# Performance work log

Measured on AMD Instinct MI355X. Metric: run time of the kernel, lower is better.

Reference implementation:

```python
import jax, jax.numpy as jnp
import numpy as np

ALP = 0.1
LAM = 1.0
N_NODES = 100000
N_EDGES = 800000
D_FEAT = 64


def setup_inputs() -> dict:
    key = jax.random.key(0)
    ks = jax.random.split(key, 7)
    h = jax.random.normal(ks[0], (N_NODES, D_FEAT), dtype=jnp.float32)
    ini_h = jax.random.normal(ks[1], (N_NODES, D_FEAT), dtype=jnp.float32)
    bef_A = jax.random.uniform(ks[2], (N_NODES, 1), dtype=jnp.float32)
    aft_A = jax.random.uniform(ks[3], (N_NODES, 1), dtype=jnp.float32)
    bef_X = jax.random.uniform(ks[4], (N_NODES, 1), dtype=jnp.float32)
    src = jax.random.randint(ks[5], (N_EDGES,), 0, N_NODES, dtype=jnp.int32)
    dst = jax.random.randint(ks[6], (N_EDGES,), 0, N_NODES, dtype=jnp.int32)
    return {"h": h, "ini_h": ini_h, "bef_A": bef_A, "aft_A": aft_A,
            "bef_X": bef_X, "src": src, "dst": dst}


def reference(h, ini_h, bef_A, aft_A, bef_X, src, dst):
    # propagation_lt:
    #   ini_h' = ini_h * bef_X
    #   agg    = A @ (h * aft_A)   (copy_u/sum over edges src->dst)
    #   out    = alp*lam * (agg * bef_A) + (1-alp)*h + alp*ini_h'
    pre_h = h
    msg = (h * aft_A)[src]                                  # [E, D]
    agg = jax.ops.segment_sum(msg, dst, num_segments=N_NODES)  # [N, D]
    agg = agg * bef_A
    return ALP * LAM * agg + (1.0 - ALP) * pre_h + ALP * (ini_h * bef_X)
```

## Files before the change

### kernel.cpp

```cpp
#include <hip/hip_runtime.h>

#define ALP 0.1f
#define OMA 0.9f
#define D 64
#define DV 16
#define SH 7
#define NODES_PER_B 128
#define NBMAX 1024
#define CAP 16
#define OVF_MAX 65536

__device__ __forceinline__ unsigned short f2b(float f) {
    unsigned u = __float_as_uint(f);
    unsigned r = u + 0x7fffu + ((u >> 16) & 1u);
    return (unsigned short)(r >> 16);
}
__device__ __forceinline__ float b2f(unsigned short u) {
    return __uint_as_float(((unsigned)u) << 16);
}

__global__ __launch_bounds__(256) void vsgc_msgp1(
        const float4* __restrict__ h4, const float* __restrict__ aft_A,
        ushort4* __restrict__ msgb, int n16,
        const int4* __restrict__ src4, const int4* __restrict__ dst4,
        int* __restrict__ gcnt, int* __restrict__ buckets,
        int2* __restrict__ ovf, int* __restrict__ ovfCnt,
        int E, int NB, int BCAP, int p1Blocks) {
    int tid = threadIdx.x;
    if ((int)blockIdx.x >= p1Blocks) {
        int i = (blockIdx.x - p1Blocks) * 256 + tid;
        if (i < n16) {
            float w = aft_A[i >> 4];
            float4 v = h4[i];
            msgb[i] = make_ushort4(f2b(v.x * w), f2b(v.y * w), f2b(v.z * w), f2b(v.w * w));
        }
        return;
    }
    __shared__ int cnt[NBMAX], gbase[NBMAX], pos[NBMAX];
#pragma unroll
    for (int j = 0; j < NBMAX / 256; ++j) { cnt[tid + j * 256] = 0; pos[tid + j * 256] = 0; }
    __syncthreads();
    int nInt4 = (E + 3) >> 2;
    int i0 = blockIdx.x * 512 + tid;
    int i1 = i0 + 256;
    bool v0 = i0 < nInt4, v1 = i1 < nInt4;
    int4 s0 = make_int4(0,0,0,0), d0 = s0, s1 = s0, d1 = s0;
    if (v0) { s0 = src4[i0]; d0 = dst4[i0]; }
    if (v1) { s1 = src4[i1]; d1 = dst4[i1]; }
    int e0 = i0 << 2, e1 = i1 << 2;
    int ss[8] = {s0.x, s0.y, s0.z, s0.w, s1.x, s1.y, s1.z, s1.w};
    int dd[8] = {d0.x, d0.y, d0.z, d0.w, d1.x, d1.y, d1.z, d1.w};
    bool ok[8];
#pragma unroll
    for (int k = 0; k < 4; ++k) { ok[k] = v0 && (e0 + k < E); ok[4 + k] = v1 && (e1 + k < E); }
#pragma unroll
    for (int k = 0; k < 8; ++k) if (ok[k]) atomicAdd(&cnt[dd[k] >> SH], 1);
    __syncthreads();
    for (int bb = tid; bb < NB; bb += 256)
        if (cnt[bb] > 0) gbase[bb] = atomicAdd(&gcnt[bb], cnt[bb]);
    __syncthreads();
    int pp[8];
#pragma unroll
    for (int k = 0; k < 8; ++k)
        pp[k] = ok[k] ? (gbase[dd[k] >> SH] + atomicAdd(&pos[dd[k] >> SH], 1)) : 0;
#pragma unroll
    for (int k = 0; k < 8; ++k) {
        if (!ok[k]) continue;
        int b = dd[k] >> SH;
        int pkt = (ss[k] << SH) | (dd[k] & (NODES_PER_B - 1));
        if (pp[k] < BCAP) buckets[(size_t)b * BCAP + pp[k]] = pkt;
        else { int o = atomicAdd(ovfCnt, 1); if (o < OVF_MAX) ovf[o] = make_int2(ss[k], dd[k]); }
    }
}

__global__ __launch_bounds__(512) void p2_gather(
        const int* __restrict__ buckets, const int* __restrict__ gcnt,
        const ushort4* __restrict__ msgb,
        const float4* __restrict__ h4, const float4* __restrict__ ini4,
        const float* __restrict__ bef_A, const float* __restrict__ bef_X,
        int2* __restrict__ ovf, int* __restrict__ ovfCnt,
        float4* __restrict__ out4, int N, int BCAP) {
    __shared__ int npos[NODES_PER_B];
    __shared__ int ells[NODES_PER_B * CAP];
    int b = blockIdx.x, tid = threadIdx.x;
    if (tid < NODES_PER_B) npos[tid] = 0;
    __syncthreads();
    int nb = min(gcnt[b], BCAP);
    const int4* bp4 = (const int4*)(buckets + (size_t)b * BCAP);
    int nIter = (nb + 3) >> 2;
    for (int i4 = tid; i4 < nIter; i4 += 512) {
        int4 r4 = bp4[i4];
        int base = i4 << 2;
        int pk[4] = {r4.x, r4.y, r4.z, r4.w};
#pragma unroll
        for (int k = 0; k < 4; ++k) {
            if (base + k >= nb) break;
            int pkt = pk[k];
            int l = pkt & (NODES_PER_B - 1);
            int s = (int)(((unsigned)pkt) >> SH);
            int slot = atomicAdd(&npos[l], 1);
            if (slot < CAP) ells[l * CAP + slot] = s;
            else { int o = atomicAdd(ovfCnt, 1); if (o < OVF_MAX) ovf[o] = make_int2(s, (b << SH) + l); }
        }
    }
    __syncthreads();
    int lane = tid & 63;
    int wv = tid >> 6;
    int w = lane >> 4;
    int q = lane & 15;
    int node0 = b << SH;
    unsigned clampN = (unsigned)(N - 1);
    for (int pair = wv; pair < NODES_PER_B / 2; pair += 8) {
        int l0 = pair * 2;
        int g0 = node0 + l0;
        if (g0 >= N) break;
        int g1 = g0 + 1;
        bool has1 = g1 < N;
        int l1c = has1 ? (l0 + 1) : l0;
        int g1c = node0 + l1c;
        size_t r0 = (size_t)g0 * DV + q;
        size_t r1 = (size_t)g1c * DV + q;
        int ev0 = ells[l0 * CAP + q];
        int ev1 = ells[l1c * CAP + q];
        int n0 = min(npos[l0], CAP);
        int n1 = has1 ? min(npos[l1c], CAP) : 0;
        float4 hv0 = h4[r0];
        float4 hv1 = h4[r1];
        float4 iv0 = ini4[r0];
        float4 iv1 = ini4[r1];
        float cb0 = ALP * bef_A[g0];
        float bx0 = ALP * bef_X[g0];
        float cb1 = ALP * bef_A[g1c];
        float bx1 = ALP * bef_X[g1c];
        float4 a0 = make_float4(0.f, 0.f, 0.f, 0.f);
        float4 a1 = a0;
#pragma unroll
        for (int k = 0; k < 4; ++k) {
            int idx = w + 4 * k;
            int s0 = __shfl(ev0, idx);
            int s1 = __shfl(ev1, idx);
            unsigned su0 = min((unsigned)s0, clampN);
            unsigned su1 = min((unsigned)s1, clampN);
            float m0 = (idx < n0) ? 1.f : 0.f;
            float m1 = (idx < n1) ? 1.f : 0.f;
            ushort4 q0 = msgb[(size_t)su0 * DV + q];
            ushort4 q1 = msgb[(size_t)su1 * DV + q];
            a0.x += m0 * b2f(q0.x); a0.y += m0 * b2f(q0.y);
            a0.z += m0 * b2f(q0.z); a0.w += m0 * b2f(q0.w);
            a1.x += m1 * b2f(q1.x); a1.y += m1 * b2f(q1.y);
            a1.z += m1 * b2f(q1.z); a1.w += m1 * b2f(q1.w);
        }
        a0.x += __shfl_xor(a0.x, 16); a0.y += __shfl_xor(a0.y, 16);
        a0.z += __shfl_xor(a0.z, 16); a0.w += __shfl_xor(a0.w, 16);
        a0.x += __shfl_xor(a0.x, 32); a0.y += __shfl_xor(a0.y, 32);
        a0.z += __shfl_xor(a0.z, 32); a0.w += __shfl_xor(a0.w, 32);
        a1.x += __shfl_xor(a1.x, 16); a1.y += __shfl_xor(a1.y, 16);
        a1.z += __shfl_xor(a1.z, 16); a1.w += __shfl_xor(a1.w, 16);
        a1.x += __shfl_xor(a1.x, 32); a1.y += __shfl_xor(a1.y, 32);
        a1.z += __shfl_xor(a1.z, 32); a1.w += __shfl_xor(a1.w, 32);
        if (w == 0) {
            float4 o;
            o.x = OMA * hv0.x + bx0 * iv0.x + cb0 * a0.x;
            o.y = OMA * hv0.y + bx0 * iv0.y + cb0 * a0.y;
            o.z = OMA * hv0.z + bx0 * iv0.z + cb0 * a0.z;
            o.w = OMA * hv0.w + bx0 * iv0.w + cb0 * a0.w;
            out4[r0] = o;
        } else if (w == 1 && has1) {
            float4 o;
            o.x = OMA * hv1.x + bx1 * iv1.x + cb1 * a1.x;
            o.y = OMA * hv1.y + bx1 * iv1.y + cb1 * a1.y;
            o.z = OMA * hv1.z + bx1 * iv1.z + cb1 * a1.z;
            o.w = OMA * hv1.w + bx1 * iv1.w + cb1 * a1.w;
            out4[r1] = o;
        }
    }
}

__global__ void vsgc_ovf(const float4* __restrict__ h4,
                         const float* __restrict__ aft_A,
                         const float* __restrict__ bef_A,
                         const int2* __restrict__ ovf,
                         const int* __restrict__ ovfCnt,
                         float* __restrict__ out) {
    int total = min(*ovfCnt, OVF_MAX);
    int stride = blockDim.x * gridDim.x;
    for (int t = blockIdx.x * blockDim.x + threadIdx.x; t < total * 16; t += stride) {
        int e = t >> 4, q = t & 15;
        int2 r = ovf[e];
        float c = ALP * aft_A[r.x] * bef_A[r.y];
        float4 hv = h4[(size_t)r.x * DV + q];
        float* op = out + (size_t)r.y * D + (q << 2);
        unsafeAtomicAdd(op + 0, c * hv.x);
        unsafeAtomicAdd(op + 1, c * hv.y);
        unsafeAtomicAdd(op + 2, c * hv.z);
        unsafeAtomicAdd(op + 3, c * hv.w);
    }
}

__global__ void vsgc_init(const float4* __restrict__ h, const float4* __restrict__ ini_h,
                          const float* __restrict__ bef_X, float4* __restrict__ out, int n4) {
    int i = blockIdx.x * blockDim.x + threadIdx.x;
    if (i >= n4) return;
    int node = i >> 4;
    float bx = ALP * bef_X[node];
    float4 hv = h[i];
    float4 iv = ini_h[i];
    float4 o;
    o.x = OMA * hv.x + bx * iv.x;
    o.y = OMA * hv.y + bx * iv.y;
    o.z = OMA * hv.z + bx * iv.z;
    o.w = OMA * hv.w + bx * iv.w;
    out[i] = o;
}
__global__ void vsgc_edges_atomic(const float4* __restrict__ h,
                                  const float* __restrict__ aft_A,
                                  const float* __restrict__ bef_A,
                                  const int* __restrict__ src,
                                  const int* __restrict__ dst,
                                  float* __restrict__ out, int E) {
    int tid = blockIdx.x * blockDim.x + threadIdx.x;
    int e = tid >> 4;
    int q = tid & 15;
    if (e >= E) return;
    int s = src[e];
    int d = dst[e];
    float c = ALP * aft_A[s] * bef_A[d];
    float4 hv = h[(size_t)s * DV + q];
    float* op = out + (size_t)d * D + (q << 2);
    unsafeAtomicAdd(op + 0, c * hv.x);
    unsafeAtomicAdd(op + 1, c * hv.y);
    unsafeAtomicAdd(op + 2, c * hv.z);
    unsafeAtomicAdd(op + 3, c * hv.w);
}

extern "C" void kernel_launch(void* const* d_in, const int* in_sizes, int n_in,
                              void* d_out, int out_size, void* d_ws, size_t ws_size,
                              hipStream_t stream) {
    const float* h     = (const float*)d_in[0];
    const float* ini_h = (const float*)d_in[1];
    const float* bef_A = (const float*)d_in[2];
    const float* aft_A = (const float*)d_in[3];
    const float* bef_X = (const float*)d_in[4];
    const int*   src   = (const int*)d_in[5];
    const int*   dst   = (const int*)d_in[6];
    float* out = (float*)d_out;

    const int N = in_sizes[0] / D;
    const int E = in_sizes[5];
    const int t = 256;

    int NB = (N + NODES_PER_B - 1) >> SH;
    int perB = (NB > 0) ? E / NB : 0;
    int BCAP = ((perB + perB / 4 + 256) + 3) & ~3;

    size_t o_gcnt = 0;
    size_t o_ovfc = NBMAX * 4;
    size_t o_ovf  = ((o_ovfc + 64 * 4 + 255) / 256) * 256;
    size_t o_bkt  = ((o_ovf + (size_t)OVF_MAX * 8 + 255) / 256) * 256;
    size_t o_msg  = ((o_bkt + (size_t)NB * BCAP * 4 + 255) / 256) * 256;
    size_t need   = o_msg + (size_t)N * 128;

    if (NB <= NBMAX && N <= (1 << (31 - SH)) && ws_size >= need) {
        int*  gcnt  = (int*)((char*)d_ws + o_gcnt);
        int*  ovfC  = (int*)((char*)d_ws + o_ovfc);
        int2* ovf   = (int2*)((char*)d_ws + o_ovf);
        int*  bkt   = (int*)((char*)d_ws + o_bkt);
        ushort4* msgb = (ushort4*)((char*)d_ws + o_msg);

        hipMemsetAsync(d_ws, 0, o_ovf, stream);

        int n16 = N * DV;
        int nInt4 = (E + 3) >> 2;
        int p1Blocks = (nInt4 + 511) / 512;
        int msgBlocks = (n16 + t - 1) / t;
        vsgc_msgp1<<<p1Blocks + msgBlocks, t, 0, stream>>>(
            (const float4*)h, aft_A, msgb, n16,
            (const int4*)src, (const int4*)dst, gcnt, bkt, ovf, ovfC,
            E, NB, BCAP, p1Blocks);

        p2_gather<<<NB, 512, 0, stream>>>(
            bkt, gcnt, msgb, (const float4*)h, (const float4*)ini_h,
            bef_A, bef_X, ovf, ovfC, (float4*)out, N, BCAP);

        vsgc_ovf<<<32, t, 0, stream>>>((const float4*)h, aft_A, bef_A, ovf, ovfC, out);
    } else {
        int n4 = N * DV;
        vsgc_init<<<(n4 + t - 1) / t, t, 0, stream>>>(
            (const float4*)h, (const float4*)ini_h, bef_X, (float4*)out, n4);
        long long total = (long long)E * DV;
        vsgc_edges_atomic<<<(int)((total + t - 1) / t), t, 0, stream>>>(
            (const float4*)h, aft_A, bef_A, src, dst, out, E);
    }
}
```

Before: 164.7 us.

## Fuse bucketing, gather and overflow passes into one cooperative persistent kernel

Replaces the memset plus three kernel launches with a single cooperative kernel that uses grid-wide syncs between phases: zeroing counters, edge bucketing, bf16 message conversion, per-bucket gather and the overflow fixup. Blocks loop persistently over edge chunks and buckets. The aim is to remove launch gaps and the memset. In exchange, the grid is capped by occupancy (at most 1024 blocks), blocks shrink from 512 to 256 threads, and the bucketing now handles 4 edges per thread per iteration, with block-level syncs inside each iteration.

```diff
diff --git a/kernel.cpp b/kernel.cpp
--- a/kernel.cpp
+++ b/kernel.cpp
@@ -1,4 +1,7 @@
 #include <hip/hip_runtime.h>
+#include <hip/hip_cooperative_groups.h>
+
+namespace cg = cooperative_groups;
 
 #define ALP 0.1f
 #define OMA 0.9f
@@ -19,181 +22,189 @@
     return __uint_as_float(((unsigned)u) << 16);
 }
 
-__global__ __launch_bounds__(256) void vsgc_msgp1(
-        const float4* __restrict__ h4, const float* __restrict__ aft_A,
-        ushort4* __restrict__ msgb, int n16,
+__global__ __launch_bounds__(256, 4) void vsgc_all(
+        const float4* __restrict__ h4, const float4* __restrict__ ini4,
+        const float* __restrict__ bef_A, const float* __restrict__ aft_A,
+        const float* __restrict__ bef_X,
         const int4* __restrict__ src4, const int4* __restrict__ dst4,
+        float4* __restrict__ out4, ushort4* __restrict__ msgb,
         int* __restrict__ gcnt, int* __restrict__ buckets,
         int2* __restrict__ ovf, int* __restrict__ ovfCnt,
-        int E, int NB, int BCAP, int p1Blocks) {
+        int N, int E, int NB, int BCAP, int n16, int nInt4) {
+    __shared__ int smraw[3 * NBMAX];
+    cg::grid_group grid = cg::this_grid();
     int tid = threadIdx.x;
-    if ((int)blockIdx.x >= p1Blocks) {
-        int i = (blockIdx.x - p1Blocks) * 256 + tid;
-        if (i < n16) {
+    int G = gridDim.x;
+
+    if (blockIdx.x == 0) {
+        for (int i = tid; i < NBMAX; i += 256) gcnt[i] = 0;
+        if (tid == 0) *ovfCnt = 0;
+    }
+    grid.sync();
+
+    {
+        int* cnt   = smraw;
+        int* gbase = smraw + NBMAX;
+        int* pos   = smraw + 2 * NBMAX;
+        for (int base4 = blockIdx.x * 256; base4 < nInt4; base4 += G * 256) {
+#pragma unroll
+            for (int j = 0; j < NBMAX / 256; ++j) { cnt[tid + j * 256] = 0; pos[tid + j * 256] = 0; }
+            __syncthreads();
+            int i4 = base4 + tid;
+            bool v = i4 < nInt4;
+            int4 sv = make_int4(0, 0, 0, 0), dv = sv;
+            if (v) { sv = src4[i4]; dv = dst4[i4]; }
+            int e0 = i4 << 2;
+            int ss[4] = {sv.x, sv.y, sv.z, sv.w};
+            int dd[4] = {dv.x, dv.y, dv.z, dv.w};
+            bool ok[4];
+#pragma unroll
+            for (int k = 0; k < 4; ++k) ok[k] = v && (e0 + k < E);
+#pragma unroll
+            for (int k = 0; k < 4; ++k) if (ok[k]) atomicAdd(&cnt[dd[k] >> SH], 1);
+            __syncthreads();
+            for (int bb = tid; bb < NB; bb += 256)
+                if (cnt[bb] > 0) gbase[bb] = atomicAdd(&gcnt[bb], cnt[bb]);
+            __syncthreads();
+            int pp[4];
+#pragma unroll
+            for (int k = 0; k < 4; ++k)
+                pp[k] = ok[k] ? (gbase[dd[k] >> SH] + atomicAdd(&pos[dd[k] >> SH], 1)) : 0;
+#pragma unroll
+            for (int k = 0; k < 4; ++k) {
+                if (!ok[k]) continue;
+                int b = dd[k] >> SH;
+                int pkt = (ss[k] << SH) | (dd[k] & (NODES_PER_B - 1));
+                if (pp[k] < BCAP) buckets[(size_t)b * BCAP + pp[k]] = pkt;
+                else { int o = atomicAdd(ovfCnt, 1); if (o < OVF_MAX) ovf[o] = make_int2(ss[k], dd[k]); }
+            }
+            __syncthreads();
+        }
+    }
+    {
+        int stride = G * 256;
+        for (int i = blockIdx.x * 256 + tid; i < n16; i += stride) {
             float w = aft_A[i >> 4];
-            float4 v = h4[i];
-            msgb[i] = make_ushort4(f2b(v.x * w), f2b(v.y * w), f2b(v.z * w), f2b(v.w * w));
+            float4 vv = h4[i];
+            msgb[i] = make_ushort4(f2b(vv.x * w), f2b(vv.y * w), f2b(vv.z * w), f2b(vv.w * w));
         }
-        return;
-    }
-    __shared__ int cnt[NBMAX], gbase[NBMAX], pos[NBMAX];
-#pragma unroll
-    for (int j = 0; j < NBMAX / 256; ++j) { cnt[tid + j * 256] = 0; pos[tid + j * 256] = 0; }
-    __syncthreads();
-    int nInt4 = (E + 3) >> 2;
-    int i0 = blockIdx.x * 512 + tid;
-    int i1 = i0 + 256;
-    bool v0 = i0 < nInt4, v1 = i1 < nInt4;
-    int4 s0 = make_int4(0,0,0,0), d0 = s0, s1 = s0, d1 = s0;
-    if (v0) { s0 = src4[i0]; d0 = dst4[i0]; }
-    if (v1) { s1 = src4[i1]; d1 = dst4[i1]; }
-    int e0 = i0 << 2, e1 = i1 << 2;
-    int ss[8] = {s0.x, s0.y, s0.z, s0.w, s1.x, s1.y, s1.z, s1.w};
-    int dd[8] = {d0.x, d0.y, d0.z, d0.w, d1.x, d1.y, d1.z, d1.w};
-    bool ok[8];
-#pragma unroll
-    for (int k = 0; k < 4; ++k) { ok[k] = v0 && (e0 + k < E); ok[4 + k] = v1 && (e1 + k < E); }
-#pragma unroll
-    for (int k = 0; k < 8; ++k) if (ok[k]) atomicAdd(&cnt[dd[k] >> SH], 1);
-    __syncthreads();
-    for (int bb = tid; bb < NB; bb += 256)
-        if (cnt[bb] > 0) gbase[bb] = atomicAdd(&gcnt[bb], cnt[bb]);
-    __syncthreads();
-    int pp[8];
-#pragma unroll
-    for (int k = 0; k < 8; ++k)
-        pp[k] = ok[k] ? (gbase[dd[k] >> SH] + atomicAdd(&pos[dd[k] >> SH], 1)) : 0;
-#pragma unroll
-    for (int k = 0; k < 8; ++k) {
-        if (!ok[k]) continue;
-        int b = dd[k] >> SH;
-        int pkt = (ss[k] << SH) | (dd[k] & (NODES_PER_B - 1));
-        if (pp[k] < BCAP) buckets[(size_t)b * BCAP + pp[k]] = pkt;
-        else { int o = atomicAdd(ovfCnt, 1); if (o < OVF_MAX) ovf[o] = make_int2(ss[k], dd[k]); }
-    }
-}
-
-__global__ __launch_bounds__(512) void p2_gather(
-        const int* __restrict__ buckets, const int* __restrict__ gcnt,
-        const ushort4* __restrict__ msgb,
-        const float4* __restrict__ h4, const float4* __restrict__ ini4,
-        const float* __restrict__ bef_A, const float* __restrict__ bef_X,
-        int2* __restrict__ ovf, int* __restrict__ ovfCnt,
-        float4* __restrict__ out4, int N, int BCAP) {
-    __shared__ int npos[NODES_PER_B];
-    __shared__ int ells[NODES_PER_B * CAP];
-    int b = blockIdx.x, tid = threadIdx.x;
-    if (tid < NODES_PER_B) npos[tid] = 0;
-    __syncthreads();
-    int nb = min(gcnt[b], BCAP);
-    const int4* bp4 = (const int4*)(buckets + (size_t)b * BCAP);
-    int nIter = (nb + 3) >> 2;
-    for (int i4 = tid; i4 < nIter; i4 += 512) {
-        int4 r4 = bp4[i4];
-        int base = i4 << 2;
-        int pk[4] = {r4.x, r4.y, r4.z, r4.w};
-#pragma unroll
-        for (int k = 0; k < 4; ++k) {
-            if (base + k >= nb) break;
-            int pkt = pk[k];
-            int l = pkt & (NODES_PER_B - 1);
-            int s = (int)(((unsigned)pkt) >> SH);
-            int slot = atomicAdd(&npos[l], 1);
-            if (slot < CAP) ells[l * CAP + slot] = s;
-            else { int o = atomicAdd(ovfCnt, 1); if (o < OVF_MAX) ovf[o] = make_int2(s, (b << SH) + l); }
+    }
+    grid.sync();
+
+    {
+        int* npos = smraw;
+        int* ells = smraw + NODES_PER_B;
+        unsigned clampN = (unsigned)(N - 1);
+        int lane = tid & 63;
+        int wv = tid >> 6;
+        int w = lane >> 4;
+        int q = lane & 15;
+        for (int b = blockIdx.x; b < NB; b += G) {
+            if (tid < NODES_PER_B) npos[tid] = 0;
+            __syncthreads();
+            int nb = min(gcnt[b], BCAP);
+            const int4* bp4 = (const int4*)(buckets + (size_t)b * BCAP);
+            int nIter = (nb + 3) >> 2;
+            for (int i4 = tid; i4 < nIter; i4 += 256) {
+                int4 r4 = bp4[i4];
+                int base = i4 << 2;
+                int pk[4] = {r4.x, r4.y, r4.z, r4.w};
+#pragma unroll
+                for (int k = 0; k < 4; ++k) {
+                    if (base + k >= nb) break;
+                    int pkt = pk[k];
+                    int l = pkt & (NODES_PER_B - 1);
+                    int s = (int)(((unsigned)pkt) >> SH);
+                    int slot = atomicAdd(&npos[l], 1);
+                    if (slot < CAP) ells[l * CAP + slot] = s;
+                    else { int o = atomicAdd(ovfCnt, 1); if (o < OVF_MAX) ovf[o] = make_int2(s, (b << SH) + l); }
+                }
+            }
+            __syncthreads();
+            int node0 = b << SH;
+            for (int pair = wv; pair < NODES_PER_B / 2; pair += 4) {
+                int l0 = pair * 2;
+                int g0 = node0 + l0;
+                if (g0 >= N) break;
+                int g1 = g0 + 1;
+                bool has1 = g1 < N;
+                int l1c = has1 ? (l0 + 1) : l0;
+                int g1c = node0 + l1c;
+                size_t r0 = (size_t)g0 * DV + q;
+                size_t r1 = (size_t)g1c * DV + q;
+                int ev0 = ells[l0 * CAP + q];
+                int ev1 = ells[l1c * CAP + q];
+                int n0 = min(npos[l0], CAP);
+                int n1 = has1 ? min(npos[l1c], CAP) : 0;
+                float4 hv0 = h4[r0];
+                float4 hv1 = h4[r1];
+                float4 iv0 = ini4[r0];
+                float4 iv1 = ini4[r1];
+                float cb0 = ALP * bef_A[g0];
+                float bx0 = ALP * bef_X[g0];
+                float cb1 = ALP * bef_A[g1c];
+                float bx1 = ALP * bef_X[g1c];
+                float4 a0 = make_float4(0.f, 0.f, 0.f, 0.f);
+                float4 a1 = a0;
+#pragma unroll
+                for (int k = 0; k < 4; ++k) {
+                    int idx = w + 4 * k;
+                    int s0 = __shfl(ev0, idx);
+                    int s1 = __shfl(ev1, idx);
+                    unsigned su0 = min((unsigned)s0, clampN);
+                    unsigned su1 = min((unsigned)s1, clampN);
+                    float m0 = (idx < n0) ? 1.f : 0.f;
+                    float m1 = (idx < n1) ? 1.f : 0.f;
+                    ushort4 q0 = msgb[(size_t)su0 * DV + q];
+                    ushort4 q1 = msgb[(size_t)su1 * DV + q];
+                    a0.x += m0 * b2f(q0.x); a0.y += m0 * b2f(q0.y);
+                    a0.z += m0 * b2f(q0.z); a0.w += m0 * b2f(q0.w);
+                    a1.x += m1 * b2f(q1.x); a1.y += m1 * b2f(q1.y);
+                    a1.z += m1 * b2f(q1.z); a1.w += m1 * b2f(q1.w);
+                }
+                a0.x += __shfl_xor(a0.x, 16); a0.y += __shfl_xor(a0.y, 16);
+                a0.z += __shfl_xor(a0.z, 16); a0.w += __shfl_xor(a0.w, 16);
+                a0.x += __shfl_xor(a0.x, 32); a0.y += __shfl_xor(a0.y, 32);
+                a0.z += __shfl_xor(a0.z, 32); a0.w += __shfl_xor(a0.w, 32);
+                a1.x += __shfl_xor(a1.x, 16); a1.y += __shfl_xor(a1.y, 16);
+                a1.z += __shfl_xor(a1.z, 16); a1.w += __shfl_xor(a1.w, 16);
+                a1.x += __shfl_xor(a1.x, 32); a1.y += __shfl_xor(a1.y, 32);
+                a1.z += __shfl_xor(a1.z, 32); a1.w += __shfl_xor(a1.w, 32);
+                if (w == 0) {
+                    float4 o;
+                    o.x = OMA * hv0.x + bx0 * iv0.x + cb0 * a0.x;
+                    o.y = OMA * hv0.y + bx0 * iv0.y + cb0 * a0.y;
+                    o.z = OMA * hv0.z + bx0 * iv0.z + cb0 * a0.z;
+                    o.w = OMA * hv0.w + bx0 * iv0.w + cb0 * a0.w;
+                    out4[r0] = o;
+                } else if (w == 1 && has1) {
+                    float4 o;
+                    o.x = OMA * hv1.x + bx1 * iv1.x + cb1 * a1.x;
+                    o.y = OMA * hv1.y + bx1 * iv1.y + cb1 * a1.y;
+                    o.z = OMA * hv1.z + bx1 * iv1.z + cb1 * a1.z;
+                    o.w = OMA * hv1.w + bx1 * iv1.w + cb1 * a1.w;
+                    out4[r1] = o;
+                }
+            }
+            __syncthreads();
         }
     }
-    __syncthreads();
-    int lane = tid & 63;
-    int wv = tid >> 6;
-    int w = lane >> 4;
-    int q = lane & 15;
-    int node0 = b << SH;
-    unsigned clampN = (unsigned)(N - 1);
-    for (int pair = wv; pair < NODES_PER_B / 2; pair += 8) {
-        int l0 = pair * 2;
-        int g0 = node0 + l0;
-        if (g0 >= N) break;
-        int g1 = g0 + 1;
-        bool has1 = g1 < N;
-        int l1c = has1 ? (l0 + 1) : l0;
-        int g1c = node0 + l1c;
-        size_t r0 = (size_t)g0 * DV + q;
-        size_t r1 = (size_t)g1c * DV + q;
-        int ev0 = ells[l0 * CAP + q];
-        int ev1 = ells[l1c * CAP + q];
-        int n0 = min(npos[l0], CAP);
-        int n1 = has1 ? min(npos[l1c], CAP) : 0;
-        float4 hv0 = h4[r0];
-        float4 hv1 = h4[r1];
-        float4 iv0 = ini4[r0];
-        float4 iv1 = ini4[r1];
-        float cb0 = ALP * bef_A[g0];
-        float bx0 = ALP * bef_X[g0];
-        float cb1 = ALP * bef_A[g1c];
-        float bx1 = ALP * bef_X[g1c];
-        float4 a0 = make_float4(0.f, 0.f, 0.f, 0.f);
-        float4 a1 = a0;
-#pragma unroll
-        for (int k = 0; k < 4; ++k) {
-            int idx = w + 4 * k;
-            int s0 = __shfl(ev0, idx);
-            int s1 = __shfl(ev1, idx);
-            unsigned su0 = min((unsigned)s0, clampN);
-            unsigned su1 = min((unsigned)s1, clampN);
-            float m0 = (idx < n0) ? 1.f : 0.f;
-            float m1 = (idx < n1) ? 1.f : 0.f;
-            ushort4 q0 = msgb[(size_t)su0 * DV + q];
-            ushort4 q1 = msgb[(size_t)su1 * DV + q];
-            a0.x += m0 * b2f(q0.x); a0.y += m0 * b2f(q0.y);
-            a0.z += m0 * b2f(q0.z); a0.w += m0 * b2f(q0.w);
-            a1.x += m1 * b2f(q1.x); a1.y += m1 * b2f(q1.y);
-            a1.z += m1 * b2f(q1.z); a1.w += m1 * b2f(q1.w);
+    grid.sync();
+
+    {
+        int total = min(*ovfCnt, OVF_MAX);
+        int stride = G * 256;
+        for (int t = blockIdx.x * 256 + tid; t < total * 16; t += stride) {
+            int e = t >> 4, qq = t & 15;
+            int2 r = ovf[e];
+            float c = ALP * aft_A[r.x] * bef_A[r.y];
+            float4 hv = h4[(size_t)r.x * DV + qq];
+            float* op = (float*)out4 + (size_t)r.y * D + (qq << 2);
+            unsafeAtomicAdd(op + 0, c * hv.x);
+            unsafeAtomicAdd(op + 1, c * hv.y);
+            unsafeAtomicAdd(op + 2, c * hv.z);
+            unsafeAtomicAdd(op + 3, c * hv.w);
         }
-        a0.x += __shfl_xor(a0.x, 16); a0.y += __shfl_xor(a0.y, 16);
-        a0.z += __shfl_xor(a0.z, 16); a0.w += __shfl_xor(a0.w, 16);
-        a0.x += __shfl_xor(a0.x, 32); a0.y += __shfl_xor(a0.y, 32);
-        a0.z += __shfl_xor(a0.z, 32); a0.w += __shfl_xor(a0.w, 32);
-        a1.x += __shfl_xor(a1.x, 16); a1.y += __shfl_xor(a1.y, 16);
-        a1.z += __shfl_xor(a1.z, 16); a1.w += __shfl_xor(a1.w, 16);
-        a1.x += __shfl_xor(a1.x, 32); a1.y += __shfl_xor(a1.y, 32);
-        a1.z += __shfl_xor(a1.z, 32); a1.w += __shfl_xor(a1.w, 32);
-        if (w == 0) {
-            float4 o;
-            o.x = OMA * hv0.x + bx0 * iv0.x + cb0 * a0.x;
-            o.y = OMA * hv0.y + bx0 * iv0.y + cb0 * a0.y;
-            o.z = OMA * hv0.z + bx0 * iv0.z + cb0 * a0.z;
-            o.w = OMA * hv0.w + bx0 * iv0.w + cb0 * a0.w;
-            out4[r0] = o;
-        } else if (w == 1 && has1) {
-            float4 o;
-            o.x = OMA * hv1.x + bx1 * iv1.x + cb1 * a1.x;
-            o.y = OMA * hv1.y + bx1 * iv1.y + cb1 * a1.y;
-            o.z = OMA * hv1.z + bx1 * iv1.z + cb1 * a1.z;
-            o.w = OMA * hv1.w + bx1 * iv1.w + cb1 * a1.w;
-            out4[r1] = o;
-        }
-    }
-}
-
-__global__ void vsgc_ovf(const float4* __restrict__ h4,
-                         const float* __restrict__ aft_A,
-                         const float* __restrict__ bef_A,
-                         const int2* __restrict__ ovf,
-                         const int* __restrict__ ovfCnt,
-                         float* __restrict__ out) {
-    int total = min(*ovfCnt, OVF_MAX);
-    int stride = blockDim.x * gridDim.x;
-    for (int t = blockIdx.x * blockDim.x + threadIdx.x; t < total * 16; t += stride) {
-        int e = t >> 4, q = t & 15;
-        int2 r = ovf[e];
-        float c = ALP * aft_A[r.x] * bef_A[r.y];
-        float4 hv = h4[(size_t)r.x * DV + q];
-        float* op = out + (size_t)r.y * D + (q << 2);
-        unsafeAtomicAdd(op + 0, c * hv.x);
-        unsafeAtomicAdd(op + 1, c * hv.y);
-        unsafeAtomicAdd(op + 2, c * hv.z);
-        unsafeAtomicAdd(op + 3, c * hv.w);
     }
 }
 
@@ -260,29 +271,45 @@
     size_t o_msg  = ((o_bkt + (size_t)NB * BCAP * 4 + 255) / 256) * 256;
     size_t need   = o_msg + (size_t)N * 128;
 
-    if (NB <= NBMAX && N <= (1 << (31 - SH)) && ws_size >= need) {
+    int dev = 0;
+    (void)hipGetDevice(&dev);
+    int coop = 0;
+    (void)hipDeviceGetAttribute(&coop, hipDeviceAttributeCooperativeLaunch, dev);
+    int numCU = 0;
+    (void)hipDeviceGetAttribute(&numCU, hipDeviceAttributeMultiprocessorCount, dev);
+    int maxBpCU = 0;
+    (void)hipOccupancyMaxActiveBlocksPerMultiprocessor(&maxBpCU, vsgc_all, 256, 0);
+
+    if (coop && numCU > 0 && maxBpCU > 0 &&
+        NB <= NBMAX && N <= (1 << (31 - SH)) && ws_size >= need) {
         int*  gcnt  = (int*)((char*)d_ws + o_gcnt);
         int*  ovfC  = (int*)((char*)d_ws + o_ovfc);
         int2* ovf   = (int2*)((char*)d_ws + o_ovf);
         int*  bkt   = (int*)((char*)d_ws + o_bkt);
         ushort4* msgb = (ushort4*)((char*)d_ws + o_msg);
 
-        hipMemsetAsync(d_ws, 0, o_ovf, stream);
-
+        long long cap = (long long)maxBpCU * numCU;
+        int G = (int)((cap < NBMAX) ? cap : NBMAX);
+
+        const float4* h4p   = (const float4*)h;
+        const float4* ini4p = (const float4*)ini_h;
+        const int4*   src4p = (const int4*)src;
+        const int4*   dst4p = (const int4*)dst;
+        float4*       out4p = (float4*)out;
+        int Nv = N, Ev = E, NBv = NB, BCAPv = BCAP;
         int n16 = N * DV;
         int nInt4 = (E + 3) >> 2;
-        int p1Blocks = (nInt4 + 511) / 512;
-        int msgBlocks = (n16 + t - 1) / t;
-        vsgc_msgp1<<<p1Blocks + msgBlocks, t, 0, stream>>>(
-            (const float4*)h, aft_A, msgb, n16,
-            (const int4*)src, (const int4*)dst, gcnt, bkt, ovf, ovfC,
-            E, NB, BCAP, p1Blocks);
-
-        p2_gather<<<NB, 512, 0, stream>>>(
-            bkt, gcnt, msgb, (const float4*)h, (const float4*)ini_h,
-            bef_A, bef_X, ovf, ovfC, (float4*)out, N, BCAP);
-
-        vsgc_ovf<<<32, t, 0, stream>>>((const float4*)h, aft_A, bef_A, ovf, ovfC, out);
+        const float* befAp = bef_A;
+        const float* aftAp = aft_A;
+        const float* befXp = bef_X;
+
+        void* args[] = {
+            (void*)&h4p, (void*)&ini4p, (void*)&befAp, (void*)&aftAp, (void*)&befXp,
+            (void*)&src4p, (void*)&dst4p, (void*)&out4p, (void*)&msgb,
+            (void*)&gcnt, (void*)&bkt, (void*)&ovf, (void*)&ovfC,
+            (void*)&Nv, (void*)&Ev, (void*)&NBv, (void*)&BCAPv, (void*)&n16, (void*)&nInt4
+        };
+        (void)hipLaunchCooperativeKernel(vsgc_all, dim3(G), dim3(256), args, 0, stream);
     } else {
         int n4 = N * DV;
         vsgc_init<<<(n4 + t - 1) / t, t, 0, stream>>>(
```

Result: slower. 429.3 us (+160.7%).

## Gather fp32 h directly and fold overflow handling into the gather kernel

Applied to the files above, without the earlier changes.

Removes the bf16 pre-scaled message buffer: the gather now reads fp32 h rows and scales each by aft_A per edge. The separate overflow kernel is dropped. Per-node slot overflow goes to a shared-memory list, global overflow entries are scanned by every block, and both are applied with atomics at the end of the same block, with a slow fallback path. This saves the msg write pass and one launch, but doubles gather bytes per edge, adds an aft_A load per edge, and makes every block scan the global overflow array.

```diff
diff --git a/kernel.cpp b/kernel.cpp
--- a/kernel.cpp
+++ b/kernel.cpp
@@ -8,35 +8,16 @@
 #define NODES_PER_B 128
 #define NBMAX 1024
 #define CAP 16
+#define OVL_CAP 512
 #define OVF_MAX 65536
 
-__device__ __forceinline__ unsigned short f2b(float f) {
-    unsigned u = __float_as_uint(f);
-    unsigned r = u + 0x7fffu + ((u >> 16) & 1u);
-    return (unsigned short)(r >> 16);
-}
-__device__ __forceinline__ float b2f(unsigned short u) {
-    return __uint_as_float(((unsigned)u) << 16);
-}
-
-__global__ __launch_bounds__(256) void vsgc_msgp1(
-        const float4* __restrict__ h4, const float* __restrict__ aft_A,
-        ushort4* __restrict__ msgb, int n16,
+__global__ __launch_bounds__(256) void vsgc_p1(
         const int4* __restrict__ src4, const int4* __restrict__ dst4,
         int* __restrict__ gcnt, int* __restrict__ buckets,
         int2* __restrict__ ovf, int* __restrict__ ovfCnt,
-        int E, int NB, int BCAP, int p1Blocks) {
+        int E, int NB, int BCAP) {
+    __shared__ int cnt[NBMAX], gbase[NBMAX], pos[NBMAX];
     int tid = threadIdx.x;
-    if ((int)blockIdx.x >= p1Blocks) {
-        int i = (blockIdx.x - p1Blocks) * 256 + tid;
-        if (i < n16) {
-            float w = aft_A[i >> 4];
-            float4 v = h4[i];
-            msgb[i] = make_ushort4(f2b(v.x * w), f2b(v.y * w), f2b(v.z * w), f2b(v.w * w));
-        }
-        return;
-    }
-    __shared__ int cnt[NBMAX], gbase[NBMAX], pos[NBMAX];
 #pragma unroll
     for (int j = 0; j < NBMAX / 256; ++j) { cnt[tid + j * 256] = 0; pos[tid + j * 256] = 0; }
     __syncthreads();
@@ -75,18 +56,22 @@
 
 __global__ __launch_bounds__(512) void p2_gather(
         const int* __restrict__ buckets, const int* __restrict__ gcnt,
-        const ushort4* __restrict__ msgb,
         const float4* __restrict__ h4, const float4* __restrict__ ini4,
-        const float* __restrict__ bef_A, const float* __restrict__ bef_X,
-        int2* __restrict__ ovf, int* __restrict__ ovfCnt,
+        const float* __restrict__ bef_A, const float* __restrict__ aft_A,
+        const float* __restrict__ bef_X,
+        const int2* __restrict__ ovf, const int* __restrict__ ovfCnt,
         float4* __restrict__ out4, int N, int BCAP) {
     __shared__ int npos[NODES_PER_B];
     __shared__ int ells[NODES_PER_B * CAP];
+    __shared__ int ovl[OVL_CAP];
+    __shared__ int novl;
     int b = blockIdx.x, tid = threadIdx.x;
     if (tid < NODES_PER_B) npos[tid] = 0;
+    if (tid == 0) novl = 0;
     __syncthreads();
     int nb = min(gcnt[b], BCAP);
     const int4* bp4 = (const int4*)(buckets + (size_t)b * BCAP);
+    const int*  bp  = buckets + (size_t)b * BCAP;
     int nIter = (nb + 3) >> 2;
     for (int i4 = tid; i4 < nIter; i4 += 512) {
         int4 r4 = bp4[i4];
@@ -97,13 +82,23 @@
             if (base + k >= nb) break;
             int pkt = pk[k];
             int l = pkt & (NODES_PER_B - 1);
-            int s = (int)(((unsigned)pkt) >> SH);
             int slot = atomicAdd(&npos[l], 1);
-            if (slot < CAP) ells[l * CAP + slot] = s;
-            else { int o = atomicAdd(ovfCnt, 1); if (o < OVF_MAX) ovf[o] = make_int2(s, (b << SH) + l); }
-        }
-    }
-    __syncthreads();
+            if (slot < CAP) ells[l * CAP + slot] = (int)(((unsigned)pkt) >> SH);
+            else { int o = atomicAdd(&novl, 1); if (o < OVL_CAP) ovl[o] = pkt; }
+        }
+    }
+    int gtot = min(*ovfCnt, OVF_MAX);
+    for (int i = tid; i < gtot; i += 512) {
+        int2 r = ovf[i];
+        if ((r.y >> SH) == b) {
+            int l = r.y & (NODES_PER_B - 1);
+            int slot = atomicAdd(&npos[l], 1);
+            if (slot < CAP) ells[l * CAP + slot] = r.x;
+            else { int o = atomicAdd(&novl, 1); if (o < OVL_CAP) ovl[o] = (r.x << SH) | l; }
+        }
+    }
+    __syncthreads();
+    bool fast = (novl <= OVL_CAP);
     int lane = tid & 63;
     int wv = tid >> 6;
     int w = lane >> 4;
@@ -122,8 +117,8 @@
         size_t r1 = (size_t)g1c * DV + q;
         int ev0 = ells[l0 * CAP + q];
         int ev1 = ells[l1c * CAP + q];
-        int n0 = min(npos[l0], CAP);
-        int n1 = has1 ? min(npos[l1c], CAP) : 0;
+        int n0 = fast ? min(npos[l0], CAP) : 0;
+        int n1 = (fast && has1) ? min(npos[l1c], CAP) : 0;
         float4 hv0 = h4[r0];
         float4 hv1 = h4[r1];
         float4 iv0 = ini4[r0];
@@ -141,14 +136,14 @@
             int s1 = __shfl(ev1, idx);
             unsigned su0 = min((unsigned)s0, clampN);
             unsigned su1 = min((unsigned)s1, clampN);
-            float m0 = (idx < n0) ? 1.f : 0.f;
-            float m1 = (idx < n1) ? 1.f : 0.f;
-            ushort4 q0 = msgb[(size_t)su0 * DV + q];
-            ushort4 q1 = msgb[(size_t)su1 * DV + q];
-            a0.x += m0 * b2f(q0.x); a0.y += m0 * b2f(q0.y);
-            a0.z += m0 * b2f(q0.z); a0.w += m0 * b2f(q0.w);
-            a1.x += m1 * b2f(q1.x); a1.y += m1 * b2f(q1.y);
-            a1.z += m1 * b2f(q1.z); a1.w += m1 * b2f(q1.w);
+            float c0 = (idx < n0) ? aft_A[su0] : 0.f;
+            float c1 = (idx < n1) ? aft_A[su1] : 0.f;
+            float4 m0 = h4[(size_t)su0 * DV + q];
+            float4 m1 = h4[(size_t)su1 * DV + q];
+            a0.x += c0 * m0.x; a0.y += c0 * m0.y;
+            a0.z += c0 * m0.z; a0.w += c0 * m0.w;
+            a1.x += c1 * m1.x; a1.y += c1 * m1.y;
+            a1.z += c1 * m1.z; a1.w += c1 * m1.w;
         }
         a0.x += __shfl_xor(a0.x, 16); a0.y += __shfl_xor(a0.y, 16);
         a0.z += __shfl_xor(a0.z, 16); a0.w += __shfl_xor(a0.w, 16);
@@ -174,26 +169,54 @@
             out4[r1] = o;
         }
     }
-}
-
-__global__ void vsgc_ovf(const float4* __restrict__ h4,
-                         const float* __restrict__ aft_A,
-                         const float* __restrict__ bef_A,
-                         const int2* __restrict__ ovf,
-                         const int* __restrict__ ovfCnt,
-                         float* __restrict__ out) {
-    int total = min(*ovfCnt, OVF_MAX);
-    int stride = blockDim.x * gridDim.x;
-    for (int t = blockIdx.x * blockDim.x + threadIdx.x; t < total * 16; t += stride) {
-        int e = t >> 4, q = t & 15;
-        int2 r = ovf[e];
-        float c = ALP * aft_A[r.x] * bef_A[r.y];
-        float4 hv = h4[(size_t)r.x * DV + q];
-        float* op = out + (size_t)r.y * D + (q << 2);
-        unsafeAtomicAdd(op + 0, c * hv.x);
-        unsafeAtomicAdd(op + 1, c * hv.y);
-        unsafeAtomicAdd(op + 2, c * hv.z);
-        unsafeAtomicAdd(op + 3, c * hv.w);
+    __syncthreads();
+    if (fast) {
+        int nov = novl;
+        int g = tid >> 4, qq = tid & 15;
+        for (int i = g; i < nov; i += 32) {
+            int pkt = ovl[i];
+            int l = pkt & (NODES_PER_B - 1);
+            int s = (int)(((unsigned)pkt) >> SH);
+            int node = node0 + l;
+            float c = ALP * bef_A[node] * aft_A[s];
+            float4 hm = h4[(size_t)s * DV + qq];
+            float* op = (float*)out4 + (size_t)node * D + (qq << 2);
+            unsafeAtomicAdd(op + 0, c * hm.x);
+            unsafeAtomicAdd(op + 1, c * hm.y);
+            unsafeAtomicAdd(op + 2, c * hm.z);
+            unsafeAtomicAdd(op + 3, c * hm.w);
+        }
+    } else {
+        for (int i = tid; i < nb; i += 512) {
+            int pkt = bp[i];
+            int l = pkt & (NODES_PER_B - 1);
+            int s = (int)(((unsigned)pkt) >> SH);
+            int node = node0 + l;
+            float c = ALP * bef_A[node] * aft_A[s];
+            const float4* hp = h4 + (size_t)s * DV;
+            float* op = (float*)out4 + (size_t)node * D;
+            for (int t = 0; t < DV; ++t) {
+                float4 hm = hp[t];
+                unsafeAtomicAdd(op + t * 4 + 0, c * hm.x);
+                unsafeAtomicAdd(op + t * 4 + 1, c * hm.y);
+                unsafeAtomicAdd(op + t * 4 + 2, c * hm.z);
+                unsafeAtomicAdd(op + t * 4 + 3, c * hm.w);
+            }
+        }
+        for (int i = tid; i < gtot; i += 512) {
+            int2 r = ovf[i];
+            if ((r.y >> SH) != b) continue;
+            float c = ALP * bef_A[r.y] * aft_A[r.x];
+            const float4* hp = h4 + (size_t)r.x * DV;
+            float* op = (float*)out4 + (size_t)r.y * D;
+            for (int t = 0; t < DV; ++t) {
+                float4 hm = hp[t];
+                unsafeAtomicAdd(op + t * 4 + 0, c * hm.x);
+                unsafeAtomicAdd(op + t * 4 + 1, c * hm.y);
+                unsafeAtomicAdd(op + t * 4 + 2, c * hm.z);
+                unsafeAtomicAdd(op + t * 4 + 3, c * hm.w);
+            }
+        }
     }
 }
 
@@ -257,32 +280,24 @@
     size_t o_ovfc = NBMAX * 4;
     size_t o_ovf  = ((o_ovfc + 64 * 4 + 255) / 256) * 256;
     size_t o_bkt  = ((o_ovf + (size_t)OVF_MAX * 8 + 255) / 256) * 256;
-    size_t o_msg  = ((o_bkt + (size_t)NB * BCAP * 4 + 255) / 256) * 256;
-    size_t need   = o_msg + (size_t)N * 128;
+    size_t need   = o_bkt + (size_t)NB * BCAP * 4;
 
     if (NB <= NBMAX && N <= (1 << (31 - SH)) && ws_size >= need) {
         int*  gcnt  = (int*)((char*)d_ws + o_gcnt);
         int*  ovfC  = (int*)((char*)d_ws + o_ovfc);
         int2* ovf   = (int2*)((char*)d_ws + o_ovf);
         int*  bkt   = (int*)((char*)d_ws + o_bkt);
-        ushort4* msgb = (ushort4*)((char*)d_ws + o_msg);
 
         hipMemsetAsync(d_ws, 0, o_ovf, stream);
 
-        int n16 = N * DV;
         int nInt4 = (E + 3) >> 2;
         int p1Blocks = (nInt4 + 511) / 512;
-        int msgBlocks = (n16 + t - 1) / t;
-        vsgc_msgp1<<<p1Blocks + msgBlocks, t, 0, stream>>>(
-            (const float4*)h, aft_A, msgb, n16,
-            (const int4*)src, (const int4*)dst, gcnt, bkt, ovf, ovfC,
-            E, NB, BCAP, p1Blocks);
+        vsgc_p1<<<p1Blocks, t, 0, stream>>>(
+            (const int4*)src, (const int4*)dst, gcnt, bkt, ovf, ovfC, E, NB, BCAP);
 
         p2_gather<<<NB, 512, 0, stream>>>(
-            bkt, gcnt, msgb, (const float4*)h, (const float4*)ini_h,
-            bef_A, bef_X, ovf, ovfC, (float4*)out, N, BCAP);
-
-        vsgc_ovf<<<32, t, 0, stream>>>((const float4*)h, aft_A, bef_A, ovf, ovfC, out);
+            bkt, gcnt, (const float4*)h, (const float4*)ini_h,
+            bef_A, aft_A, bef_X, ovf, ovfC, (float4*)out, N, BCAP);
     } else {
         int n4 = N * DV;
         vsgc_init<<<(n4 + t - 1) / t, t, 0, stream>>>(
```

Result: faster. 160.0 us (-2.8%).
